# Optimization experiments

Hardware: AMD Instinct MI355X
Metric: run time of the kernel (lower is better)

The kernel has to match this reference:

```python
import jax, jax.numpy as jnp
import numpy as np

NUM_HEADS = 12


def _rope(t, cos, sin):
    # t: (B, H, M, D); cos/sin: (M, D//2) applied to interleaved pairs
    B, H, M, D = t.shape
    t2 = t.reshape(B, H, M, D // 2, 2)
    t0, t1 = t2[..., 0], t2[..., 1]
    c = cos[None, None]  # (1,1,M,D//2)
    s = sin[None, None]
    r0 = t0 * c - t1 * s
    r1 = t0 * s + t1 * c
    return jnp.stack([r0, r1], axis=-1).reshape(B, H, M, D)


def setup_inputs() -> dict:
    key = jax.random.key(0)
    ks = jax.random.split(key, 7)
    B, N, C = 16, 577, 768
    Hd = C // NUM_HEADS
    x = jax.random.normal(ks[0], (B, N, C), dtype=jnp.float32)
    # rotary angles for N-1 non-CLS tokens
    theta = jax.random.uniform(ks[1], (N - 1, Hd // 2), dtype=jnp.float32) * 6.28318
    cos = jnp.cos(theta)
    sin = jnp.sin(theta)
    w_qkv = jax.random.normal(ks[2], (C, 3 * C), dtype=jnp.float32) * 0.02
    b_qkv = jax.random.normal(ks[3], (3 * C,), dtype=jnp.float32) * 0.02
    w_proj = jax.random.normal(ks[4], (C, C), dtype=jnp.float32) * 0.02
    b_proj = jax.random.normal(ks[5], (C,), dtype=jnp.float32) * 0.02
    return {"x": x, "cos": cos, "sin": sin, "w_qkv": w_qkv, "b_qkv": b_qkv,
            "w_proj": w_proj, "b_proj": b_proj}


def reference(x, cos, sin, w_qkv, b_qkv, w_proj, b_proj):
    B, N, C = x.shape
    H = NUM_HEADS
    D = C // H
    scale = D ** -0.5
    qkv = x @ w_qkv + b_qkv                       # (B, N, 3C)
    qkv = qkv.reshape(B, N, 3, H, D).transpose(2, 0, 3, 1, 4)  # (3, B, H, N, D)
    q, k, v = qkv[0], qkv[1], qkv[2]
    # RoPE applied to all tokens except the CLS token (index 0)
    q = jnp.concatenate([q[:, :, :1], _rope(q[:, :, 1:], cos, sin)], axis=2)
    k = jnp.concatenate([k[:, :, :1], _rope(k[:, :, 1:], cos, sin)], axis=2)
    attn = jax.nn.softmax(jnp.einsum('bhnd,bhmd->bhnm', q, k) * scale, axis=-1)
    out = jnp.einsum('bhnm,bhmd->bhnd', attn, v)  # (B, H, N, D)
    out = out.transpose(0, 2, 1, 3).reshape(B, N, C)
    return out @ w_proj + b_proj
```

## Files before the change

### kernel.cpp

```cpp
#include <hip/hip_runtime.h>
#include <stdint.h>

typedef unsigned short u16;
typedef __attribute__((ext_vector_type(8))) short bf16x8;
typedef __attribute__((ext_vector_type(4))) float f32x4;

#define MFMA16(a, b, c) __builtin_amdgcn_mfma_f32_16x16x32_bf16((a), (b), (c), 0, 0, 0)

__device__ __forceinline__ float b2f(u16 u) {
    union { unsigned int i; float f; } v; v.i = ((unsigned int)u) << 16; return v.f;
}
__device__ __forceinline__ u16 f2b(float f) {
    union { float f; unsigned int i; } v; v.f = f;
    unsigned int r = v.i + 0x7fffu + ((v.i >> 16) & 1u);
    return (u16)(r >> 16);
}

typedef __attribute__((address_space(1))) void gvoid;
typedef __attribute__((address_space(3))) void lvoid;
__device__ __forceinline__ void gld16(const void* g, void* l) {
    __builtin_amdgcn_global_load_lds((gvoid*)(void*)g, (lvoid*)l, 16, 0, 0);
}

__device__ __forceinline__ void tile_from_bid(int bid, int nTM, int nTN,
                                              int& rt, int& ct) {
    const int PW = 8;
    const int full = nTM / PW;
    const int per = PW * nTN;
    int p = bid / per;
    int pw = PW;
    int rem = bid - p * per;
    if (p >= full) { p = full; rem = bid - full * per; pw = nTM - full * PW; }
    const int c = rem / pw;
    const int r = rem - c * pw;
    rt = p * PW + r;
    ct = c;
}

__global__ __launch_bounds__(256) void f32_to_bf16(const float* __restrict__ in,
                                                   u16* __restrict__ out, int n) {
    const int i = (blockIdx.x * 256 + threadIdx.x) * 4;
    if (i + 3 < n) {
        const float4 v = *(const float4*)(in + i);
        ushort4 o;
        o.x = f2b(v.x); o.y = f2b(v.y); o.z = f2b(v.z); o.w = f2b(v.w);
        *(ushort4*)(out + i) = o;
    }
}

__global__ __launch_bounds__(256) void transpose_w(const float* __restrict__ wqkv,
                                                   const float* __restrict__ wproj,
                                                   u16* __restrict__ outQ,
                                                   u16* __restrict__ outP) {
    __shared__ float tile[32][33];
    int bx = blockIdx.x;
    const float* in; u16* out; int C;
    if (bx < 72) { in = wqkv; out = outQ; C = 2304; }
    else         { bx -= 72; in = wproj; out = outP; C = 768; }
    const int R = 768;
    const int t = threadIdx.x;
    const int r = t >> 3, c4 = (t & 7) * 4;
    const int ir = blockIdx.y * 32 + r, ic = bx * 32 + c4;
    const float4 v = *(const float4*)(in + (size_t)ir * C + ic);
    tile[r][c4 + 0] = v.x; tile[r][c4 + 1] = v.y;
    tile[r][c4 + 2] = v.z; tile[r][c4 + 3] = v.w;
    __syncthreads();
    const int orow = bx * 32 + r, ocol = blockIdx.y * 32 + c4;
    ushort4 o;
    o.x = f2b(tile[c4 + 0][r]); o.y = f2b(tile[c4 + 1][r]);
    o.z = f2b(tile[c4 + 2][r]); o.w = f2b(tile[c4 + 3][r]);
    *(ushort4*)(out + (size_t)orow * R + ocol) = o;
}

template <int EPI>
__global__ __launch_bounds__(512) void gemm_bt(const u16* __restrict__ A,
                                               const u16* __restrict__ Bt,
                                               const float* __restrict__ bias,
                                               void* __restrict__ Cv,
                                               const float* __restrict__ cosp,
                                               const float* __restrict__ sinp,
                                               u16* __restrict__ VtG,
                                               int M, int N, int K) {
    __shared__ __align__(16) u16 As0[128 * 64];
    __shared__ __align__(16) u16 As1[128 * 64];
    __shared__ __align__(16) u16 Bs0[128 * 64];
    __shared__ __align__(16) u16 Bs1[128 * 64];

    const int t = threadIdx.x;
    const int lane = t & 63;
    const int wave = t >> 6;
    const int l15 = lane & 15, quad = lane >> 4;
    const int wm = wave >> 2;
    const int wn = wave & 3;

    int rt, ct;
    tile_from_bid(blockIdx.y * gridDim.x + blockIdx.x, gridDim.x, gridDim.y, rt, ct);
    const int row0 = rt * 128;
    const int col0 = ct * 128;

    const f32x4 fz = {0.f, 0.f, 0.f, 0.f};
    f32x4 acc[4][2];
#pragma unroll
    for (int i = 0; i < 4; ++i)
#pragma unroll
        for (int j = 0; j < 2; ++j) acc[i][j] = fz;

    const u16* Ap[2];
    const u16* Bp[2];
    int off[2];
#pragma unroll
    for (int n = 0; n < 2; ++n) {
        const int g = t + n * 512;
        const int row = g >> 3;
        const int slot = (g & 7) ^ (row & 7);
        int ar = row0 + row; if (ar > M - 1) ar = M - 1;
        Ap[n] = A + (size_t)ar * K + slot * 8;
        Bp[n] = Bt + (size_t)(col0 + row) * K + slot * 8;
        off[n] = g * 8;
    }

#define STAGE(kt_, Ad, Bd) do {                                            \
        const int kb_ = (kt_) << 6;                                        \
        gld16(Ap[0] + kb_, (Ad) + off[0]);                                 \
        gld16(Ap[1] + kb_, (Ad) + off[1]);                                 \
        gld16(Bp[0] + kb_, (Bd) + off[0]);                                 \
        gld16(Bp[1] + kb_, (Bd) + off[1]);                                 \
    } while (0)

#define COMPUTE(Asb, Bsb) do {                                             \
        _Pragma("unroll")                                                  \
        for (int kk = 0; kk < 2; ++kk) {                                   \
            const int swk = ((kk * 4 + quad) ^ (l15 & 7)) * 8;             \
            bf16x8 af[4], bfr[2];                                          \
            _Pragma("unroll")                                              \
            for (int mi = 0; mi < 4; ++mi)                                 \
                af[mi] = *(const bf16x8*)((Asb) +                          \
                    ((wm * 4 + mi) * 16 + l15) * 64 + swk);                \
            _Pragma("unroll")                                              \
            for (int ni = 0; ni < 2; ++ni)                                 \
                bfr[ni] = *(const bf16x8*)((Bsb) +                         \
                    ((wn * 2 + ni) * 16 + l15) * 64 + swk);                \
            _Pragma("unroll")                                              \
            for (int mi = 0; mi < 4; ++mi)                                 \
                _Pragma("unroll")                                          \
                for (int ni = 0; ni < 2; ++ni)                             \
                    acc[mi][ni] = MFMA16(bfr[ni], af[mi], acc[mi][ni]);    \
        }                                                                  \
    } while (0)

    const int nKT = K >> 6;
    STAGE(0, As0, Bs0);
    __syncthreads();

    for (int kt = 0; kt < nKT; kt += 2) {
        if (kt + 1 < nKT) STAGE(kt + 1, As1, Bs1);
        COMPUTE(As0, Bs0);
        __syncthreads();
        if (kt + 2 < nKT) STAGE(kt + 2, As0, Bs0);
        COMPUTE(As1, Bs1);
        __syncthreads();
    }
#undef STAGE
#undef COMPUTE

    if (EPI == 2) {
        if (col0 >= 1536) {
#pragma unroll
            for (int mi = 0; mi < 4; ++mi) {
                const int row = row0 + wm * 64 + mi * 16 + l15;
                if (row < M) {
                    const int bb = row / 577, n = row - bb * 577;
                    u16* vdst = VtG + (size_t)bb * 491520 + n;
#pragma unroll
                    for (int ni = 0; ni < 2; ++ni) {
                        const int colb = col0 + wn * 32 + ni * 16 + quad * 4;
                        const float4 bv = *(const float4*)(bias + colb);
#pragma unroll
                        for (int r = 0; r < 4; ++r) {
                            const int cv = colb + r - 1536;
                            vdst[(size_t)(cv >> 6) * 40960 + (cv & 63) * 640] =
                                f2b(acc[mi][ni][r] + ((const float*)&bv)[r]);
                        }
                    }
                }
            }
        } else {
#pragma unroll
            for (int mi = 0; mi < 4; ++mi) {
                const int row = row0 + wm * 64 + mi * 16 + l15;
                if (row < M) {
                    const int bb = row / 577, n = row - bb * 577;
                    const bool hr = (n >= 1);
                    const float* cb = cosp + (size_t)(hr ? (n - 1) : 0) * 32;
                    const float* sb = sinp + (size_t)(hr ? (n - 1) : 0) * 32;
                    u16* outp = (u16*)Cv + (size_t)row * 1536;
#pragma unroll
                    for (int ni = 0; ni < 2; ++ni) {
                        const int colb = col0 + wn * 32 + ni * 16 + quad * 4;
                        const float4 bv = *(const float4*)(bias + colb);
                        const int pi = (colb & 63) >> 1;
                        float2 c = *(const float2*)(cb + pi);
                        float2 s = *(const float2*)(sb + pi);
                        if (!hr) { c.x = 1.f; c.y = 1.f; s.x = 0.f; s.y = 0.f; }
                        const float v0 = acc[mi][ni][0] + bv.x;
                        const float v1 = acc[mi][ni][1] + bv.y;
                        const float v2 = acc[mi][ni][2] + bv.z;
                        const float v3 = acc[mi][ni][3] + bv.w;
                        ushort4 o;
                        o.x = f2b(v0 * c.x - v1 * s.x);
                        o.y = f2b(v0 * s.x + v1 * c.x);
                        o.z = f2b(v2 * c.y - v3 * s.y);
                        o.w = f2b(v2 * s.y + v3 * c.y);
                        *(ushort4*)(outp + colb) = o;
                    }
                }
            }
        }
    } else {
#pragma unroll
        for (int ni = 0; ni < 2; ++ni) {
            const int colb = col0 + wn * 32 + ni * 16 + quad * 4;
            const float4 bv = *(const float4*)(bias + colb);
#pragma unroll
            for (int mi = 0; mi < 4; ++mi) {
                const int row = row0 + wm * 64 + mi * 16 + l15;
                if (row < M) {
                    float4 o;
                    o.x = acc[mi][ni][0] + bv.x; o.y = acc[mi][ni][1] + bv.y;
                    o.z = acc[mi][ni][2] + bv.z; o.w = acc[mi][ni][3] + bv.w;
                    *(float4*)((float*)Cv + (size_t)row * N + colb) = o;
                }
            }
        }
    }
}

#define PSTR 72

__global__ __launch_bounds__(256) void attn2(const u16* __restrict__ qkv,
                                             const u16* __restrict__ VtG,
                                             u16* __restrict__ aout) {
    __shared__ __align__(16) u16 Ks[64 * 64];
    __shared__ __align__(16) u16 Vs[64 * 64];
    __shared__ __align__(16) u16 Pb[4 * 16 * PSTR];

    const int t = threadIdx.x;
    const int lane = t & 63, wave = t >> 6;
    const int l15 = lane & 15, quad = lane >> 4;
    const int qt = blockIdx.x;
    const int bh = blockIdx.y;
    const int b = bh / 12, h = bh - b * 12;
    const u16* baseQ = qkv + (size_t)b * 577 * 1536 + h * 64;
    const u16* baseK = baseQ + 768;
    const u16* vbase = VtG + (size_t)bh * 64 * 640;

    const int mq = qt * 64 + wave * 16 + l15;
    const int nq = mq < 577 ? mq : 576;
    bf16x8 aq[2];
    aq[0] = *(const bf16x8*)(baseQ + (size_t)nq * 1536 + quad * 8);
    aq[1] = *(const bf16x8*)(baseQ + (size_t)nq * 1536 + 32 + quad * 8);

    const int r15 = t & 15, cc = (t >> 4) & 7, rg0 = t >> 7;
    const int row0 = rg0 * 16 + r15, row1 = row0 + 32;
    u16* kl0 = Ks + t * 8;  u16* kl1 = Ks + (t + 256) * 8;
    u16* vl0 = Vs + t * 8;  u16* vl1 = Vs + (t + 256) * 8;
    const u16* vp0 = vbase + (size_t)row0 * 640 + cc * 8;
    const u16* vp1 = vbase + (size_t)row1 * 640 + cc * 8;

    u16* Pw = Pb + wave * 16 * PSTR;

    f32x4 oacc[4];
    const f32x4 fz = {0.f, 0.f, 0.f, 0.f};
#pragma unroll
    for (int i = 0; i < 4; ++i) oacc[i] = fz;
    float m4[4] = {-1e30f, -1e30f, -1e30f, -1e30f};
    float l4[4] = {0.f, 0.f, 0.f, 0.f};

    for (int kt = 0; kt < 10; ++kt) {
        __syncthreads();
        {
            int n0 = kt * 64 + row0; if (n0 > 576) n0 = 576;
            int n1 = kt * 64 + row1; if (n1 > 576) n1 = 576;
            gld16(baseK + (size_t)n0 * 1536 + cc * 8, kl0);
            gld16(baseK + (size_t)n1 * 1536 + cc * 8, kl1);
            gld16(vp0 + kt * 64, vl0);
            gld16(vp1 + kt * 64, vl1);
        }
        __syncthreads();

        f32x4 sacc[4];
#pragma unroll
        for (int nt = 0; nt < 4; ++nt) {
            sacc[nt] = fz;
#pragma unroll
            for (int kk = 0; kk < 2; ++kk) {
                const bf16x8 bk = *(const bf16x8*)(Ks + (nt * 128 + (kk * 4 + quad) * 16 + l15) * 8);
                sacc[nt] = MFMA16(aq[kk], bk, sacc[nt]);
            }
        }
        float sv[4][4];
#pragma unroll
        for (int nt = 0; nt < 4; ++nt) {
            const int key = kt * 64 + nt * 16 + l15;
            const bool kvalid = key < 577;
#pragma unroll
            for (int r = 0; r < 4; ++r)
                sv[nt][r] = kvalid ? sacc[nt][r] * 0.125f : -1e30f;
        }
        float mt[4];
#pragma unroll
        for (int r = 0; r < 4; ++r) {
            mt[r] = fmaxf(fmaxf(sv[0][r], sv[1][r]), fmaxf(sv[2][r], sv[3][r]));
#pragma unroll
            for (int off = 1; off <= 8; off <<= 1)
                mt[r] = fmaxf(mt[r], __shfl_xor(mt[r], off));
        }
        float alpha[4];
#pragma unroll
        for (int r = 0; r < 4; ++r) {
            const float mnew = fmaxf(m4[r], mt[r]);
            alpha[r] = __expf(m4[r] - mnew);
            m4[r] = mnew;
        }
        float lsum[4] = {0.f, 0.f, 0.f, 0.f};
#pragma unroll
        for (int nt = 0; nt < 4; ++nt) {
#pragma unroll
            for (int r = 0; r < 4; ++r) {
                const float p = __expf(sv[nt][r] - m4[r]);
                lsum[r] += p;
                Pw[(quad * 4 + r) * PSTR + nt * 16 + l15] = f2b(p);
            }
        }
#pragma unroll
        for (int r = 0; r < 4; ++r) {
#pragma unroll
            for (int off = 1; off <= 8; off <<= 1)
                lsum[r] += __shfl_xor(lsum[r], off);
            l4[r] = l4[r] * alpha[r] + lsum[r];
        }
#pragma unroll
        for (int dt = 0; dt < 4; ++dt)
#pragma unroll
            for (int r = 0; r < 4; ++r) oacc[dt][r] *= alpha[r];

        __asm__ __volatile__("s_waitcnt lgkmcnt(0)" ::: "memory");

#pragma unroll
        for (int kc = 0; kc < 2; ++kc) {
            const bf16x8 pf = *(const bf16x8*)(Pw + l15 * PSTR + kc * 32 + quad * 8);
#pragma unroll
            for (int dt = 0; dt < 4; ++dt) {
                const bf16x8 vf = *(const bf16x8*)(Vs + (dt * 128 + (kc * 4 + quad) * 16 + l15) * 8);
                oacc[dt] = MFMA16(pf, vf, oacc[dt]);
            }
        }
    }

    float linv[4];
#pragma unroll
    for (int r = 0; r < 4; ++r) linv[r] = 1.f / l4[r];
#pragma unroll
    for (int r = 0; r < 4; ++r) {
        const int n = qt * 64 + wave * 16 + quad * 4 + r;
        if (n < 577) {
            u16* op = aout + ((size_t)b * 577 + n) * 768 + h * 64 + l15;
#pragma unroll
            for (int dt = 0; dt < 4; ++dt)
                op[dt * 16] = f2b(oacc[dt][r] * linv[r]);
        }
    }
}

extern "C" void kernel_launch(void* const* d_in, const int* in_sizes, int n_in,
                              void* d_out, int out_size, void* d_ws, size_t ws_size,
                              hipStream_t stream) {
    const float* x      = (const float*)d_in[0];
    const float* cosp   = (const float*)d_in[1];
    const float* sinp   = (const float*)d_in[2];
    const float* w_qkv  = (const float*)d_in[3];
    const float* b_qkv  = (const float*)d_in[4];
    const float* w_proj = (const float*)d_in[5];
    const float* b_proj = (const float*)d_in[6];
    float* out = (float*)d_out;

    char* ws = (char*)d_ws;
    u16* xb     = (u16*)(ws);
    u16* aout   = (u16*)(ws);
    u16* wqkvT  = (u16*)(ws + 14180352);
    u16* wprojT = (u16*)(ws + 17719296);
    u16* qkv    = (u16*)(ws + 18898944);
    u16* VtG    = (u16*)(ws + 47259648);

    f32_to_bf16<<<6924, 256, 0, stream>>>(x, xb, 7090176);
    transpose_w<<<dim3(96, 24), 256, 0, stream>>>(w_qkv, w_proj, wqkvT, wprojT);
    gemm_bt<2><<<dim3(73, 18), 512, 0, stream>>>(xb, wqkvT, b_qkv, qkv,
                                                 cosp, sinp, VtG, 9232, 2304, 768);
    attn2<<<dim3(10, 192), 256, 0, stream>>>(qkv, VtG, aout);
    gemm_bt<1><<<dim3(73, 6), 512, 0, stream>>>(aout, wprojT, b_proj, out,
                                                nullptr, nullptr, nullptr, 9232, 768, 768);
}
```

Measured before the change: 243.4 us.

## Double-buffer K/V tiles in attention with XOR-swizzled LDS and exp2 softmax

The attention kernel now uses two LDS buffers for K and V, so the next tile's global-to-LDS load is issued while the current tile is computed, and the loop is unrolled in pairs with a specialised masked final tile. LDS rows are XOR-swizzled to avoid bank conflicts on fragment reads. Softmax uses a raw v_exp_f32 (exp2) with the scale folded into a single FMA constant. The grid is flattened to 1D with a block swizzle that spreads consecutive blocks across heads. This uses more LDS per block, which may reduce occupancy. The final tile reuses row 576 for K but reads past it for V, relying on masking.

```diff
diff --git a/kernel.cpp b/kernel.cpp
--- a/kernel.cpp
+++ b/kernel.cpp
@@ -14,6 +14,9 @@
     union { float f; unsigned int i; } v; v.f = f;
     unsigned int r = v.i + 0x7fffu + ((v.i >> 16) & 1u);
     return (u16)(r >> 16);
+}
+__device__ __forceinline__ float exp2_fast(float x) {
+    float r; __asm__("v_exp_f32 %0, %1" : "=v"(r) : "v"(x)); return r;
 }
 
 typedef __attribute__((address_space(1))) void gvoid;
@@ -236,19 +239,24 @@
 }
 
 #define PSTR 72
+#define CEXP 0.18033688011112042f
 
 __global__ __launch_bounds__(256) void attn2(const u16* __restrict__ qkv,
                                              const u16* __restrict__ VtG,
                                              u16* __restrict__ aout) {
-    __shared__ __align__(16) u16 Ks[64 * 64];
-    __shared__ __align__(16) u16 Vs[64 * 64];
+    __shared__ __align__(16) u16 Ks0[64 * 64];
+    __shared__ __align__(16) u16 Ks1[64 * 64];
+    __shared__ __align__(16) u16 Vs0[64 * 64];
+    __shared__ __align__(16) u16 Vs1[64 * 64];
     __shared__ __align__(16) u16 Pb[4 * 16 * PSTR];
 
     const int t = threadIdx.x;
     const int lane = t & 63, wave = t >> 6;
     const int l15 = lane & 15, quad = lane >> 4;
-    const int qt = blockIdx.x;
-    const int bh = blockIdx.y;
+
+    const int bid = blockIdx.x;
+    const int swz = (bid & 7) * 240 + (bid >> 3);
+    const int bh = swz / 10, qt = swz - bh * 10;
     const int b = bh / 12, h = bh - b * 12;
     const u16* baseQ = qkv + (size_t)b * 577 * 1536 + h * 64;
     const u16* baseK = baseQ + 768;
@@ -260,12 +268,19 @@
     aq[0] = *(const bf16x8*)(baseQ + (size_t)nq * 1536 + quad * 8);
     aq[1] = *(const bf16x8*)(baseQ + (size_t)nq * 1536 + 32 + quad * 8);
 
-    const int r15 = t & 15, cc = (t >> 4) & 7, rg0 = t >> 7;
-    const int row0 = rg0 * 16 + r15, row1 = row0 + 32;
-    u16* kl0 = Ks + t * 8;  u16* kl1 = Ks + (t + 256) * 8;
-    u16* vl0 = Vs + t * 8;  u16* vl1 = Vs + (t + 256) * 8;
-    const u16* vp0 = vbase + (size_t)row0 * 640 + cc * 8;
-    const u16* vp1 = vbase + (size_t)row1 * 640 + cc * 8;
+    const int g0 = t, g1 = t + 256;
+    const int r0 = g0 >> 3, r1 = g1 >> 3;
+    const int s0 = (g0 & 7) ^ (r0 & 7), s1 = (g1 & 7) ^ (r1 & 7);
+    const int o0 = g0 * 8, o1 = g1 * 8;
+    const u16* Kp0 = baseK + (size_t)r0 * 1536 + s0 * 8;
+    const u16* Kp1 = baseK + (size_t)r1 * 1536 + s1 * 8;
+    const u16* Vp0 = vbase + (size_t)r0 * 640 + s0 * 8;
+    const u16* Vp1 = vbase + (size_t)r1 * 640 + s1 * 8;
+    const u16* K9p0 = baseK + (size_t)576 * 1536 + s0 * 8;
+    const u16* K9p1 = baseK + (size_t)576 * 1536 + s1 * 8;
+
+    const int swk0 = (quad ^ (l15 & 7)) * 8;
+    const int swk1 = ((4 + quad) ^ (l15 & 7)) * 8;
 
     u16* Pw = Pb + wave * 16 * PSTR;
 
@@ -276,86 +291,107 @@
     float m4[4] = {-1e30f, -1e30f, -1e30f, -1e30f};
     float l4[4] = {0.f, 0.f, 0.f, 0.f};
 
-    for (int kt = 0; kt < 10; ++kt) {
+#define ASTAGE(kt_, Kd, Vd) do {                                            \
+        gld16(Kp0 + (size_t)(kt_) * 98304, (Kd) + o0);                      \
+        gld16(Kp1 + (size_t)(kt_) * 98304, (Kd) + o1);                      \
+        gld16(Vp0 + (kt_) * 64, (Vd) + o0);                                 \
+        gld16(Vp1 + (kt_) * 64, (Vd) + o1);                                 \
+    } while (0)
+
+#define ASTAGE9(Kd, Vd) do {                                                \
+        gld16(K9p0, (Kd) + o0);                                             \
+        gld16(K9p1, (Kd) + o1);                                             \
+        gld16(Vp0 + 576, (Vd) + o0);                                        \
+        gld16(Vp1 + 576, (Vd) + o1);                                        \
+    } while (0)
+
+#define ATT_TILE(kt_, Kb, Vb, MASKED) do {                                  \
+        f32x4 sacc[4];                                                      \
+        _Pragma("unroll")                                                   \
+        for (int nt = 0; nt < 4; ++nt) {                                    \
+            sacc[nt] = fz;                                                  \
+            const bf16x8 bk0 = *(const bf16x8*)((Kb) + (nt * 16 + l15) * 64 + swk0); \
+            sacc[nt] = MFMA16(aq[0], bk0, sacc[nt]);                        \
+            const bf16x8 bk1 = *(const bf16x8*)((Kb) + (nt * 16 + l15) * 64 + swk1); \
+            sacc[nt] = MFMA16(aq[1], bk1, sacc[nt]);                        \
+        }                                                                   \
+        float sv[4][4];                                                     \
+        _Pragma("unroll")                                                   \
+        for (int nt = 0; nt < 4; ++nt)                                      \
+            _Pragma("unroll")                                               \
+            for (int r = 0; r < 4; ++r) {                                   \
+                float s_ = sacc[nt][r];                                     \
+                if (MASKED && ((kt_) * 64 + nt * 16 + l15 > 576)) s_ = -1e30f; \
+                sv[nt][r] = s_;                                             \
+            }                                                               \
+        float mt[4];                                                        \
+        _Pragma("unroll")                                                   \
+        for (int r = 0; r < 4; ++r) {                                       \
+            mt[r] = fmaxf(fmaxf(sv[0][r], sv[1][r]), fmaxf(sv[2][r], sv[3][r])); \
+            _Pragma("unroll")                                               \
+            for (int off = 1; off <= 8; off <<= 1)                          \
+                mt[r] = fmaxf(mt[r], __shfl_xor(mt[r], off));               \
+        }                                                                   \
+        float alpha[4], nmc[4];                                             \
+        _Pragma("unroll")                                                   \
+        for (int r = 0; r < 4; ++r) {                                       \
+            const float mnew = fmaxf(m4[r], mt[r]);                         \
+            alpha[r] = exp2_fast((m4[r] - mnew) * CEXP);                    \
+            m4[r] = mnew;                                                   \
+            nmc[r] = -mnew * CEXP;                                          \
+        }                                                                   \
+        float lsum[4] = {0.f, 0.f, 0.f, 0.f};                               \
+        _Pragma("unroll")                                                   \
+        for (int nt = 0; nt < 4; ++nt)                                      \
+            _Pragma("unroll")                                               \
+            for (int r = 0; r < 4; ++r) {                                   \
+                const float p = exp2_fast(__builtin_fmaf(sv[nt][r], CEXP, nmc[r])); \
+                lsum[r] += p;                                               \
+                Pw[(quad * 4 + r) * PSTR + nt * 16 + l15] = f2b(p);         \
+            }                                                               \
+        _Pragma("unroll")                                                   \
+        for (int r = 0; r < 4; ++r) {                                       \
+            _Pragma("unroll")                                               \
+            for (int off = 1; off <= 8; off <<= 1)                          \
+                lsum[r] += __shfl_xor(lsum[r], off);                        \
+            l4[r] = l4[r] * alpha[r] + lsum[r];                             \
+        }                                                                   \
+        _Pragma("unroll")                                                   \
+        for (int dt = 0; dt < 4; ++dt)                                      \
+            _Pragma("unroll")                                               \
+            for (int r = 0; r < 4; ++r) oacc[dt][r] *= alpha[r];            \
+        __asm__ __volatile__("s_waitcnt lgkmcnt(0)" ::: "memory");          \
+        _Pragma("unroll")                                                   \
+        for (int kc = 0; kc < 2; ++kc) {                                    \
+            const bf16x8 pf = *(const bf16x8*)(Pw + l15 * PSTR + kc * 32 + quad * 8); \
+            const int swkv = kc ? swk1 : swk0;                              \
+            _Pragma("unroll")                                               \
+            for (int dt = 0; dt < 4; ++dt) {                                \
+                const bf16x8 vf = *(const bf16x8*)((Vb) + (dt * 16 + l15) * 64 + swkv); \
+                oacc[dt] = MFMA16(pf, vf, oacc[dt]);                        \
+            }                                                               \
+        }                                                                   \
+    } while (0)
+
+    ASTAGE(0, Ks0, Vs0);
+    __syncthreads();
+
+    for (int kt2 = 0; kt2 < 8; kt2 += 2) {
+        ASTAGE(kt2 + 1, Ks1, Vs1);
+        ATT_TILE(kt2, Ks0, Vs0, false);
         __syncthreads();
-        {
-            int n0 = kt * 64 + row0; if (n0 > 576) n0 = 576;
-            int n1 = kt * 64 + row1; if (n1 > 576) n1 = 576;
-            gld16(baseK + (size_t)n0 * 1536 + cc * 8, kl0);
-            gld16(baseK + (size_t)n1 * 1536 + cc * 8, kl1);
-            gld16(vp0 + kt * 64, vl0);
-            gld16(vp1 + kt * 64, vl1);
-        }
+        ASTAGE(kt2 + 2, Ks0, Vs0);
+        ATT_TILE(kt2 + 1, Ks1, Vs1, false);
         __syncthreads();
-
-        f32x4 sacc[4];
-#pragma unroll
-        for (int nt = 0; nt < 4; ++nt) {
-            sacc[nt] = fz;
-#pragma unroll
-            for (int kk = 0; kk < 2; ++kk) {
-                const bf16x8 bk = *(const bf16x8*)(Ks + (nt * 128 + (kk * 4 + quad) * 16 + l15) * 8);
-                sacc[nt] = MFMA16(aq[kk], bk, sacc[nt]);
-            }
-        }
-        float sv[4][4];
-#pragma unroll
-        for (int nt = 0; nt < 4; ++nt) {
-            const int key = kt * 64 + nt * 16 + l15;
-            const bool kvalid = key < 577;
-#pragma unroll
-            for (int r = 0; r < 4; ++r)
-                sv[nt][r] = kvalid ? sacc[nt][r] * 0.125f : -1e30f;
-        }
-        float mt[4];
-#pragma unroll
-        for (int r = 0; r < 4; ++r) {
-            mt[r] = fmaxf(fmaxf(sv[0][r], sv[1][r]), fmaxf(sv[2][r], sv[3][r]));
-#pragma unroll
-            for (int off = 1; off <= 8; off <<= 1)
-                mt[r] = fmaxf(mt[r], __shfl_xor(mt[r], off));
-        }
-        float alpha[4];
-#pragma unroll
-        for (int r = 0; r < 4; ++r) {
-            const float mnew = fmaxf(m4[r], mt[r]);
-            alpha[r] = __expf(m4[r] - mnew);
-            m4[r] = mnew;
-        }
-        float lsum[4] = {0.f, 0.f, 0.f, 0.f};
-#pragma unroll
-        for (int nt = 0; nt < 4; ++nt) {
-#pragma unroll
-            for (int r = 0; r < 4; ++r) {
-                const float p = __expf(sv[nt][r] - m4[r]);
-                lsum[r] += p;
-                Pw[(quad * 4 + r) * PSTR + nt * 16 + l15] = f2b(p);
-            }
-        }
-#pragma unroll
-        for (int r = 0; r < 4; ++r) {
-#pragma unroll
-            for (int off = 1; off <= 8; off <<= 1)
-                lsum[r] += __shfl_xor(lsum[r], off);
-            l4[r] = l4[r] * alpha[r] + lsum[r];
-        }
-#pragma unroll
-        for (int dt = 0; dt < 4; ++dt)
-#pragma unroll
-            for (int r = 0; r < 4; ++r) oacc[dt][r] *= alpha[r];
-
-        __asm__ __volatile__("s_waitcnt lgkmcnt(0)" ::: "memory");
-
-#pragma unroll
-        for (int kc = 0; kc < 2; ++kc) {
-            const bf16x8 pf = *(const bf16x8*)(Pw + l15 * PSTR + kc * 32 + quad * 8);
-#pragma unroll
-            for (int dt = 0; dt < 4; ++dt) {
-                const bf16x8 vf = *(const bf16x8*)(Vs + (dt * 128 + (kc * 4 + quad) * 16 + l15) * 8);
-                oacc[dt] = MFMA16(pf, vf, oacc[dt]);
-            }
-        }
-    }
+    }
+    ASTAGE9(Ks1, Vs1);
+    ATT_TILE(8, Ks0, Vs0, false);
+    __syncthreads();
+    ATT_TILE(9, Ks1, Vs1, true);
+
+#undef ASTAGE
+#undef ASTAGE9
+#undef ATT_TILE
 
     float linv[4];
 #pragma unroll
@@ -396,7 +432,7 @@
     transpose_w<<<dim3(96, 24), 256, 0, stream>>>(w_qkv, w_proj, wqkvT, wprojT);
     gemm_bt<2><<<dim3(73, 18), 512, 0, stream>>>(xb, wqkvT, b_qkv, qkv,
                                                  cosp, sinp, VtG, 9232, 2304, 768);
-    attn2<<<dim3(10, 192), 256, 0, stream>>>(qkv, VtG, aout);
+    attn2<<<dim3(1920), 256, 0, stream>>>(qkv, VtG, aout);
     gemm_bt<1><<<dim3(73, 6), 512, 0, stream>>>(aout, wprojT, b_proj, out,
                                                 nullptr, nullptr, nullptr, 9232, 768, 768);
 }
```

Result: faster. 229.6 us (-5.7%).
